# Kernel tuning notes

Measured on AMD Instinct MI355X. Metric: run time of the kernel, lower is better.

The kernel has to match this reference:

```python
import jax, jax.numpy as jnp
import numpy as np

# Conv config matching init_kwargs
C_IN, C_OUT = 128, 256
KH, KW = 3, 3
STRIDE = (1, 1)
PADDING = ((1, 1), (1, 1))
DILATION = (1, 1)
B, H, W = 32, 56, 56


def setup_inputs() -> dict:
    key = jax.random.key(0)
    k1, k2, k3 = jax.random.split(key, 3)
    x = jax.random.normal(k1, (B, C_IN, H, W), dtype=jnp.float32)
    # Flattened weight as stored by Conv2DUF: conv.weight.view(O,-1).t() -> [C*kh*kw, O]
    weight = jax.random.normal(k2, (C_IN * KH * KW, C_OUT), dtype=jnp.float32) * 0.02
    bias = jax.random.normal(k3, (C_OUT,), dtype=jnp.float32) * 0.02
    return {"x": x, "weight": weight, "bias": bias}


def reference(x, weight, bias):
    # Conv2DUF computes unfold(x) @ weight + bias, which is exactly a 2D
    # cross-correlation with the original conv kernel. Recover the [O,C,kh,kw]
    # kernel from the flattened [C*kh*kw, O] matrix and use the fused conv
    # primitive (same math, no giant im2col buffer).
    kernel = weight.T.reshape(C_OUT, C_IN, KH, KW)
    out = jax.lax.conv_general_dilated(
        x, kernel,
        window_strides=STRIDE,
        padding=PADDING,
        rhs_dilation=DILATION,
        dimension_numbers=("NCHW", "OIHW", "NCHW"),
    )
    return out + bias[None, :, None, None]
```

## Files before the change

kernel.cpp:

```cpp
#include <hip/hip_runtime.h>
#include <stdint.h>


#define C_INQ 128
#define C_OUTQ 256
#define HDIM 56
#define WDIM 56
#define BDIM 32
#define HP 58
#define WP 58
#define HWPIX (HDIM * WDIM)
#define GSTRIDE (BDIM * HP * WP * 8)
#define XT_ELEMS ((size_t)16 * GSTRIDE)
#define XT_BYTES (XT_ELEMS * 2)

typedef __bf16 bf16x8 __attribute__((ext_vector_type(8)));
typedef unsigned short ushort8 __attribute__((ext_vector_type(8)));
typedef float floatx4 __attribute__((ext_vector_type(4)));

__device__ __forceinline__ unsigned short f2bf(float f) {
  union { float f; unsigned int u; } v; v.f = f;
  unsigned int u = v.u;
  unsigned int r = u + 0x7FFFu + ((u >> 16) & 1u);
  return (unsigned short)(r >> 16);
}
__device__ __forceinline__ unsigned int pack2(float a, float b) {
  return (unsigned int)f2bf(a) | ((unsigned int)f2bf(b) << 16);
}

__global__ __launch_bounds__(256) void pad_transpose_kernel(
    const float* __restrict__ x, unsigned short* __restrict__ xt) {
  const int blk = blockIdx.x;
  const int b = blk / HP;
  const int hp = blk - b * HP;
  const int t = threadIdx.x;
  uint4* __restrict__ xt4 = (uint4*)xt;
  if (hp == 0 || hp == HP - 1) {
    for (int i = t; i < 16 * WP; i += 256) {
      int g = i / WP, wp = i - g * WP;
      xt4[((size_t)(g * BDIM + b) * HP + hp) * WP + wp] = make_uint4(0, 0, 0, 0);
    }
    return;
  }
  const int h = hp - 1;
  if (t < 224) {
    const int g = t / 14;
    const int w4 = (t - g * 14) * 4;
    const float* xp = x + ((size_t)b * C_INQ + g * 8) * HWPIX + h * WDIM + w4;
    float4 L0 = *(const float4*)(xp);
    float4 L1 = *(const float4*)(xp + HWPIX);
    float4 L2 = *(const float4*)(xp + 2 * HWPIX);
    float4 L3 = *(const float4*)(xp + 3 * HWPIX);
    float4 L4 = *(const float4*)(xp + 4 * HWPIX);
    float4 L5 = *(const float4*)(xp + 5 * HWPIX);
    float4 L6 = *(const float4*)(xp + 6 * HWPIX);
    float4 L7 = *(const float4*)(xp + 7 * HWPIX);
    uint4* dst = xt4 + ((size_t)(g * BDIM + b) * HP + hp) * WP + 1 + w4;
    dst[0] = make_uint4(pack2(L0.x, L1.x), pack2(L2.x, L3.x),
                        pack2(L4.x, L5.x), pack2(L6.x, L7.x));
    dst[1] = make_uint4(pack2(L0.y, L1.y), pack2(L2.y, L3.y),
                        pack2(L4.y, L5.y), pack2(L6.y, L7.y));
    dst[2] = make_uint4(pack2(L0.z, L1.z), pack2(L2.z, L3.z),
                        pack2(L4.z, L5.z), pack2(L6.z, L7.z));
    dst[3] = make_uint4(pack2(L0.w, L1.w), pack2(L2.w, L3.w),
                        pack2(L4.w, L5.w), pack2(L6.w, L7.w));
  } else {
    const int r = t - 224;
    const int g = r >> 1;
    const int wp = (r & 1) * (WP - 1);
    xt4[((size_t)(g * BDIM + b) * HP + hp) * WP + wp] = make_uint4(0, 0, 0, 0);
  }
}

__global__ __launch_bounds__(256) void weight_transform_kernel(
    const float* __restrict__ w, unsigned short* __restrict__ wt) {
  const int bx = blockIdx.x;
  const int khw = bx >> 4;
  const int r4 = bx & 15;
  const int n0w = (r4 >> 2) * 64;
  const int c32 = (r4 & 3) * 32;
  const int t = threadIdx.x;
  __shared__ float lds[32 * 66];
#pragma unroll
  for (int r = 0; r < 8; ++r) {
    int idx = r * 256 + t;
    int n = idx & 63, c = idx >> 6;
    lds[c * 66 + n] = w[(size_t)((c32 + c) * 9 + khw) * C_OUTQ + n0w + n];
  }
  __syncthreads();
  {
    int n = t >> 2, c8 = (t & 3) * 8;
    const float* s = lds + c8 * 66 + n;
    uint4 o;
    o.x = pack2(s[0],   s[66]);
    o.y = pack2(s[132], s[198]);
    o.z = pack2(s[264], s[330]);
    o.w = pack2(s[396], s[462]);
    *(uint4*)(wt + (size_t)khw * (C_OUTQ * C_INQ) + (size_t)(n0w + n) * C_INQ + c32 + c8) = o;
  }
}

#define BM 128
#define BN 256
#define BK 32
#define STEPS 36

__global__ __launch_bounds__(256, 2) void conv_gemm_kernel(
    const unsigned short* __restrict__ xt,
    const unsigned short* __restrict__ wt,
    const float* __restrict__ bias,
    float* __restrict__ out) {
  __shared__ __align__(16) unsigned short ldsA[3 * BM * BK];
  __shared__ __align__(16) unsigned short ldsB[3 * BN * BK];

  const int t = threadIdx.x;
  const int lane = t & 63;
  const int wave = t >> 6;
  const int tile_m = blockIdx.x;

  int gbaseA[2], gbaseB[4];
#pragma unroll
  for (int r = 0; r < 2; ++r) {
    int g = r * 256 + t;
    int row = g >> 2;
    int kpart = (g & 3) ^ (row & 3);
    int pix = tile_m * BM + row;
    int b = pix / HWPIX;
    int p = pix - b * HWPIX;
    int h = p / WDIM;
    int w = p - h * WDIM;
    gbaseA[r] = kpart * GSTRIDE + ((b * HP + h) * WP + w) * 8;
  }
#pragma unroll
  for (int r = 0; r < 4; ++r) {
    int g = r * 256 + t;
    int row = g >> 2;
    int kpart = (g & 3) ^ (row & 3);
    gbaseB[r] = row * C_INQ + kpart * 8;
  }

  const int wm = (wave >> 1) * 64;
  const int wn = (wave & 1) * 128;
  const int mrow = lane & 15;
  const int quad = lane >> 4;

  int aoff[4], boff[8];
#pragma unroll
  for (int i = 0; i < 4; ++i) {
    int row = wm + i * 16 + mrow;
    aoff[i] = row * BK + ((quad ^ (row & 3)) * 8);
  }
#pragma unroll
  for (int j = 0; j < 8; ++j) {
    int row = wn + j * 16 + mrow;
    boff[j] = row * BK + ((quad ^ (row & 3)) * 8);
  }

  const int ldst = wave * 64 * 8;

  floatx4 acc[4][8] = {};

  auto stage = [&](int s2, int bufc) {
    const int khw = s2 >> 2;
    const int cq = s2 & 3;
    const int kh = khw / 3;
    const int kw = khw - kh * 3;
    const int koffA = cq * 4 * GSTRIDE + (kh * WP + kw) * 8;
    const int koffB = khw * (C_OUTQ * C_INQ) + cq * 32;
#pragma unroll
    for (int r = 0; r < 2; ++r)
      __builtin_amdgcn_global_load_lds(
          (const __attribute__((address_space(1))) unsigned int*)(xt + gbaseA[r] + koffA),
          (__attribute__((address_space(3))) unsigned int*)(ldsA + bufc * (BM * BK) + r * 2048 + ldst),
          16, 0, 0);
#pragma unroll
    for (int r = 0; r < 4; ++r)
      __builtin_amdgcn_global_load_lds(
          (const __attribute__((address_space(1))) unsigned int*)(wt + gbaseB[r] + koffB),
          (__attribute__((address_space(3))) unsigned int*)(ldsB + bufc * (BN * BK) + r * 2048 + ldst),
          16, 0, 0);
  };

  auto compute_step = [&](int bufc) {
    const unsigned short* A = ldsA + bufc * (BM * BK);
    const unsigned short* B = ldsB + bufc * (BN * BK);
    bf16x8 afr[4], bfr[8];
#pragma unroll
    for (int i = 0; i < 4; ++i)
      afr[i] = __builtin_bit_cast(bf16x8, *(const ushort8*)(A + aoff[i]));
#pragma unroll
    for (int j = 0; j < 8; ++j)
      bfr[j] = __builtin_bit_cast(bf16x8, *(const ushort8*)(B + boff[j]));
#pragma unroll
    for (int i = 0; i < 4; ++i)
#pragma unroll
      for (int j = 0; j < 8; ++j)
        acc[i][j] = __builtin_amdgcn_mfma_f32_16x16x32_bf16(afr[i], bfr[j], acc[i][j], 0, 0, 0);
  };

#define K_STEP(S, BUF, VM, DOSTAGE)                                  \
  {                                                                  \
    asm volatile("s_waitcnt vmcnt(" VM ")" ::: "memory");            \
    __builtin_amdgcn_s_barrier();                                    \
    compute_step(BUF);                                               \
    __builtin_amdgcn_s_barrier();                                    \
    if (DOSTAGE) stage((S) + 3, BUF);                                \
  }

  stage(0, 0);
  stage(1, 1);
  stage(2, 2);

#pragma unroll 1
  for (int so = 0; so < 11; ++so) {
    const int s = so * 3;
    K_STEP(s, 0, "12", true);
    K_STEP(s + 1, 1, "12", true);
    K_STEP(s + 2, 2, "12", true);
  }
  K_STEP(33, 0, "12", false);
  K_STEP(34, 1, "6", false);
  K_STEP(35, 2, "0", false);
#undef K_STEP

  float bv[8];
#pragma unroll
  for (int jn = 0; jn < 8; ++jn) bv[jn] = bias[wn + jn * 16 + mrow];
#pragma unroll
  for (int i = 0; i < 4; ++i) {
    const int mbase = tile_m * BM + wm + i * 16 + quad * 4;
    const int b = mbase / HWPIX;
    const int p = mbase - b * HWPIX;
    float* obase = out + (size_t)b * (C_OUTQ * HWPIX) + p;
#pragma unroll
    for (int jn = 0; jn < 8; ++jn) {
      const int ng = wn + jn * 16 + mrow;
      floatx4 v = acc[i][jn];
      v[0] += bv[jn]; v[1] += bv[jn]; v[2] += bv[jn]; v[3] += bv[jn];
      *(floatx4*)(obase + (size_t)ng * HWPIX) = v;
    }
  }
}

extern "C" void kernel_launch(void* const* d_in, const int* in_sizes, int n_in,
                              void* d_out, int out_size, void* d_ws, size_t ws_size,
                              hipStream_t stream) {
  const float* x    = (const float*)d_in[0];
  const float* w    = (const float*)d_in[1];
  const float* bias = (const float*)d_in[2];
  float* out = (float*)d_out;

  unsigned short* xt = (unsigned short*)d_ws;
  unsigned short* wt = (unsigned short*)((char*)d_ws + XT_BYTES);

  hipLaunchKernelGGL(pad_transpose_kernel, dim3(BDIM * HP), dim3(256), 0, stream, x, xt);
  hipLaunchKernelGGL(weight_transform_kernel, dim3(144), dim3(256), 0, stream, w, wt);
  hipLaunchKernelGGL(conv_gemm_kernel, dim3(784), dim3(256), 0, stream, xt, wt, bias, out);
}
```

Baseline: 234.4 us.

## Enlarge GEMM tile to 256x256x64 with 8 waves and merge prep kernels

New measurement: 232.1 us. Within noise of the previous version (-1.0%).

```diff
diff --git a/kernel.cpp b/kernel.cpp
--- a/kernel.cpp
+++ b/kernel.cpp
@@ -28,102 +28,102 @@
   return (unsigned int)f2bf(a) | ((unsigned int)f2bf(b) << 16);
 }
 
-__global__ __launch_bounds__(256) void pad_transpose_kernel(
-    const float* __restrict__ x, unsigned short* __restrict__ xt) {
-  const int blk = blockIdx.x;
-  const int b = blk / HP;
-  const int hp = blk - b * HP;
+#define PAD_BLOCKS (BDIM * HP)
+__global__ __launch_bounds__(256) void prep_kernel(
+    const float* __restrict__ x, unsigned short* __restrict__ xt,
+    const float* __restrict__ w, unsigned short* __restrict__ wt) {
   const int t = threadIdx.x;
-  uint4* __restrict__ xt4 = (uint4*)xt;
-  if (hp == 0 || hp == HP - 1) {
-    for (int i = t; i < 16 * WP; i += 256) {
-      int g = i / WP, wp = i - g * WP;
+  if (blockIdx.x < PAD_BLOCKS) {
+    const int blk = blockIdx.x;
+    const int b = blk / HP;
+    const int hp = blk - b * HP;
+    uint4* __restrict__ xt4 = (uint4*)xt;
+    if (hp == 0 || hp == HP - 1) {
+      for (int i = t; i < 16 * WP; i += 256) {
+        int g = i / WP, wp = i - g * WP;
+        xt4[((size_t)(g * BDIM + b) * HP + hp) * WP + wp] = make_uint4(0, 0, 0, 0);
+      }
+      return;
+    }
+    const int h = hp - 1;
+    if (t < 224) {
+      const int g = t / 14;
+      const int w4 = (t - g * 14) * 4;
+      const float* xp = x + ((size_t)b * C_INQ + g * 8) * HWPIX + h * WDIM + w4;
+      float4 L0 = *(const float4*)(xp);
+      float4 L1 = *(const float4*)(xp + HWPIX);
+      float4 L2 = *(const float4*)(xp + 2 * HWPIX);
+      float4 L3 = *(const float4*)(xp + 3 * HWPIX);
+      float4 L4 = *(const float4*)(xp + 4 * HWPIX);
+      float4 L5 = *(const float4*)(xp + 5 * HWPIX);
+      float4 L6 = *(const float4*)(xp + 6 * HWPIX);
+      float4 L7 = *(const float4*)(xp + 7 * HWPIX);
+      uint4* dst = xt4 + ((size_t)(g * BDIM + b) * HP + hp) * WP + 1 + w4;
+      dst[0] = make_uint4(pack2(L0.x, L1.x), pack2(L2.x, L3.x),
+                          pack2(L4.x, L5.x), pack2(L6.x, L7.x));
+      dst[1] = make_uint4(pack2(L0.y, L1.y), pack2(L2.y, L3.y),
+                          pack2(L4.y, L5.y), pack2(L6.y, L7.y));
+      dst[2] = make_uint4(pack2(L0.z, L1.z), pack2(L2.z, L3.z),
+                          pack2(L4.z, L5.z), pack2(L6.z, L7.z));
+      dst[3] = make_uint4(pack2(L0.w, L1.w), pack2(L2.w, L3.w),
+                          pack2(L4.w, L5.w), pack2(L6.w, L7.w));
+    } else {
+      const int r = t - 224;
+      const int g = r >> 1;
+      const int wp = (r & 1) * (WP - 1);
       xt4[((size_t)(g * BDIM + b) * HP + hp) * WP + wp] = make_uint4(0, 0, 0, 0);
     }
-    return;
-  }
-  const int h = hp - 1;
-  if (t < 224) {
-    const int g = t / 14;
-    const int w4 = (t - g * 14) * 4;
-    const float* xp = x + ((size_t)b * C_INQ + g * 8) * HWPIX + h * WDIM + w4;
-    float4 L0 = *(const float4*)(xp);
-    float4 L1 = *(const float4*)(xp + HWPIX);
-    float4 L2 = *(const float4*)(xp + 2 * HWPIX);
-    float4 L3 = *(const float4*)(xp + 3 * HWPIX);
-    float4 L4 = *(const float4*)(xp + 4 * HWPIX);
-    float4 L5 = *(const float4*)(xp + 5 * HWPIX);
-    float4 L6 = *(const float4*)(xp + 6 * HWPIX);
-    float4 L7 = *(const float4*)(xp + 7 * HWPIX);
-    uint4* dst = xt4 + ((size_t)(g * BDIM + b) * HP + hp) * WP + 1 + w4;
-    dst[0] = make_uint4(pack2(L0.x, L1.x), pack2(L2.x, L3.x),
-                        pack2(L4.x, L5.x), pack2(L6.x, L7.x));
-    dst[1] = make_uint4(pack2(L0.y, L1.y), pack2(L2.y, L3.y),
-                        pack2(L4.y, L5.y), pack2(L6.y, L7.y));
-    dst[2] = make_uint4(pack2(L0.z, L1.z), pack2(L2.z, L3.z),
-                        pack2(L4.z, L5.z), pack2(L6.z, L7.z));
-    dst[3] = make_uint4(pack2(L0.w, L1.w), pack2(L2.w, L3.w),
-                        pack2(L4.w, L5.w), pack2(L6.w, L7.w));
   } else {
-    const int r = t - 224;
-    const int g = r >> 1;
-    const int wp = (r & 1) * (WP - 1);
-    xt4[((size_t)(g * BDIM + b) * HP + hp) * WP + wp] = make_uint4(0, 0, 0, 0);
-  }
-}
-
-__global__ __launch_bounds__(256) void weight_transform_kernel(
-    const float* __restrict__ w, unsigned short* __restrict__ wt) {
-  const int bx = blockIdx.x;
-  const int khw = bx >> 4;
-  const int r4 = bx & 15;
-  const int n0w = (r4 >> 2) * 64;
-  const int c32 = (r4 & 3) * 32;
-  const int t = threadIdx.x;
-  __shared__ float lds[32 * 66];
-#pragma unroll
-  for (int r = 0; r < 8; ++r) {
-    int idx = r * 256 + t;
-    int n = idx & 63, c = idx >> 6;
-    lds[c * 66 + n] = w[(size_t)((c32 + c) * 9 + khw) * C_OUTQ + n0w + n];
-  }
-  __syncthreads();
-  {
-    int n = t >> 2, c8 = (t & 3) * 8;
-    const float* s = lds + c8 * 66 + n;
-    uint4 o;
-    o.x = pack2(s[0],   s[66]);
-    o.y = pack2(s[132], s[198]);
-    o.z = pack2(s[264], s[330]);
-    o.w = pack2(s[396], s[462]);
-    *(uint4*)(wt + (size_t)khw * (C_OUTQ * C_INQ) + (size_t)(n0w + n) * C_INQ + c32 + c8) = o;
-  }
-}
-
-#define BM 128
+    const int bx = blockIdx.x - PAD_BLOCKS;
+    const int khw = bx >> 4;
+    const int r4 = bx & 15;
+    const int n0w = (r4 >> 2) * 64;
+    const int c32 = (r4 & 3) * 32;
+    __shared__ float lds[32 * 66];
+#pragma unroll
+    for (int r = 0; r < 8; ++r) {
+      int idx = r * 256 + t;
+      int n = idx & 63, c = idx >> 6;
+      lds[c * 66 + n] = w[(size_t)((c32 + c) * 9 + khw) * C_OUTQ + n0w + n];
+    }
+    __syncthreads();
+    {
+      int n = t >> 2, c8 = (t & 3) * 8;
+      const float* s = lds + c8 * 66 + n;
+      uint4 o;
+      o.x = pack2(s[0],   s[66]);
+      o.y = pack2(s[132], s[198]);
+      o.z = pack2(s[264], s[330]);
+      o.w = pack2(s[396], s[462]);
+      *(uint4*)(wt + (size_t)khw * (C_OUTQ * C_INQ) + (size_t)(n0w + n) * C_INQ + c32 + c8) = o;
+    }
+  }
+}
+
+#define BM 256
 #define BN 256
-#define BK 32
-#define STEPS 36
-
-__global__ __launch_bounds__(256, 2) void conv_gemm_kernel(
+#define BK 64
+#define NT 18
+
+__global__ __launch_bounds__(512, 2) void conv_gemm_kernel(
     const unsigned short* __restrict__ xt,
     const unsigned short* __restrict__ wt,
     const float* __restrict__ bias,
     float* __restrict__ out) {
-  __shared__ __align__(16) unsigned short ldsA[3 * BM * BK];
-  __shared__ __align__(16) unsigned short ldsB[3 * BN * BK];
+  __shared__ __align__(16) unsigned short ldsA[2 * BM * BK];
+  __shared__ __align__(16) unsigned short ldsB[2 * BN * BK];
 
   const int t = threadIdx.x;
   const int lane = t & 63;
   const int wave = t >> 6;
   const int tile_m = blockIdx.x;
 
-  int gbaseA[2], gbaseB[4];
-#pragma unroll
-  for (int r = 0; r < 2; ++r) {
-    int g = r * 256 + t;
-    int row = g >> 2;
-    int kpart = (g & 3) ^ (row & 3);
+  int gbaseA[4], gbaseB[4];
+#pragma unroll
+  for (int r = 0; r < 4; ++r) {
+    int g = r * 512 + t;
+    int row = g >> 3;
+    int kpart = (g & 7) ^ (row & 7);
     int pix = tile_m * BM + row;
     int b = pix / HWPIX;
     int p = pix - b * HWPIX;
@@ -133,110 +133,111 @@
   }
 #pragma unroll
   for (int r = 0; r < 4; ++r) {
-    int g = r * 256 + t;
-    int row = g >> 2;
-    int kpart = (g & 3) ^ (row & 3);
-    gbaseB[r] = row * C_INQ + kpart * 8;
-  }
-
-  const int wm = (wave >> 1) * 64;
-  const int wn = (wave & 1) * 128;
+    int g = r * 512 + t;
+    int n = g >> 3;
+    int kpart = (g & 7) ^ (n & 7);
+    gbaseB[r] = n * C_INQ + kpart * 8;
+  }
+
+  const int wm = (wave >> 2) * 128;
+  const int wn = (wave & 3) * 64;
   const int mrow = lane & 15;
   const int quad = lane >> 4;
-
-  int aoff[4], boff[8];
-#pragma unroll
-  for (int i = 0; i < 4; ++i) {
-    int row = wm + i * 16 + mrow;
-    aoff[i] = row * BK + ((quad ^ (row & 3)) * 8);
-  }
-#pragma unroll
-  for (int j = 0; j < 8; ++j) {
-    int row = wn + j * 16 + mrow;
-    boff[j] = row * BK + ((quad ^ (row & 3)) * 8);
-  }
-
-  const int ldst = wave * 64 * 8;
-
-  floatx4 acc[4][8] = {};
-
-  auto stage = [&](int s2, int bufc) {
-    const int khw = s2 >> 2;
-    const int cq = s2 & 3;
+  const int xorv = mrow & 7;
+  const int kx0 = (quad ^ xorv) * 8;
+  const int kx1 = ((4 + quad) ^ xorv) * 8;
+
+  floatx4 acc[8][4] = {};
+
+  auto stage = [&](int kt, int buf) {
+    const int khw = kt >> 1;
+    const int chalf = kt & 1;
     const int kh = khw / 3;
     const int kw = khw - kh * 3;
-    const int koffA = cq * 4 * GSTRIDE + (kh * WP + kw) * 8;
-    const int koffB = khw * (C_OUTQ * C_INQ) + cq * 32;
-#pragma unroll
-    for (int r = 0; r < 2; ++r)
+    const int koffA = chalf * 8 * GSTRIDE + (kh * WP + kw) * 8;
+    const int koffB = khw * (C_OUTQ * C_INQ) + chalf * 64;
+    const int ldst = t * 8;
+#pragma unroll
+    for (int r = 0; r < 4; ++r)
       __builtin_amdgcn_global_load_lds(
           (const __attribute__((address_space(1))) unsigned int*)(xt + gbaseA[r] + koffA),
-          (__attribute__((address_space(3))) unsigned int*)(ldsA + bufc * (BM * BK) + r * 2048 + ldst),
+          (__attribute__((address_space(3))) unsigned int*)(ldsA + buf * (BM * BK) + r * 4096 + ldst),
           16, 0, 0);
 #pragma unroll
     for (int r = 0; r < 4; ++r)
       __builtin_amdgcn_global_load_lds(
           (const __attribute__((address_space(1))) unsigned int*)(wt + gbaseB[r] + koffB),
-          (__attribute__((address_space(3))) unsigned int*)(ldsB + bufc * (BN * BK) + r * 2048 + ldst),
+          (__attribute__((address_space(3))) unsigned int*)(ldsB + buf * (BN * BK) + r * 4096 + ldst),
           16, 0, 0);
   };
 
-  auto compute_step = [&](int bufc) {
-    const unsigned short* A = ldsA + bufc * (BM * BK);
-    const unsigned short* B = ldsB + bufc * (BN * BK);
-    bf16x8 afr[4], bfr[8];
-#pragma unroll
-    for (int i = 0; i < 4; ++i)
-      afr[i] = __builtin_bit_cast(bf16x8, *(const ushort8*)(A + aoff[i]));
-#pragma unroll
-    for (int j = 0; j < 8; ++j)
-      bfr[j] = __builtin_bit_cast(bf16x8, *(const ushort8*)(B + boff[j]));
-#pragma unroll
-    for (int i = 0; i < 4; ++i)
-#pragma unroll
-      for (int j = 0; j < 8; ++j)
-        acc[i][j] = __builtin_amdgcn_mfma_f32_16x16x32_bf16(afr[i], bfr[j], acc[i][j], 0, 0, 0);
+  auto compute_tile = [&](int buf) {
+    const unsigned short* A = ldsA + buf * (BM * BK);
+    const unsigned short* B = ldsB + buf * (BN * BK);
+    bf16x8 bfr[4][2];
+#pragma unroll
+    for (int j = 0; j < 4; ++j) {
+      const unsigned short* br = B + (wn + j * 16 + mrow) * BK;
+      bfr[j][0] = __builtin_bit_cast(bf16x8, *(const ushort8*)(br + kx0));
+      bfr[j][1] = __builtin_bit_cast(bf16x8, *(const ushort8*)(br + kx1));
+    }
+#pragma unroll
+    for (int p = 0; p < 4; ++p) {
+      bf16x8 af[2][2];
+#pragma unroll
+      for (int i2 = 0; i2 < 2; ++i2) {
+        const unsigned short* ar = A + (wm + (p * 2 + i2) * 16 + mrow) * BK;
+        af[i2][0] = __builtin_bit_cast(bf16x8, *(const ushort8*)(ar + kx0));
+        af[i2][1] = __builtin_bit_cast(bf16x8, *(const ushort8*)(ar + kx1));
+      }
+      __builtin_amdgcn_s_setprio(1);
+#pragma unroll
+      for (int i2 = 0; i2 < 2; ++i2)
+#pragma unroll
+        for (int u = 0; u < 2; ++u)
+#pragma unroll
+          for (int j = 0; j < 4; ++j)
+            acc[p * 2 + i2][j] = __builtin_amdgcn_mfma_f32_16x16x32_bf16(
+                af[i2][u], bfr[j][u], acc[p * 2 + i2][j], 0, 0, 0);
+      __builtin_amdgcn_s_setprio(0);
+    }
   };
 
-#define K_STEP(S, BUF, VM, DOSTAGE)                                  \
+#define K_STEP(T, BUF, VM, DOSTAGE)                                  \
   {                                                                  \
     asm volatile("s_waitcnt vmcnt(" VM ")" ::: "memory");            \
     __builtin_amdgcn_s_barrier();                                    \
-    compute_step(BUF);                                               \
+    compute_tile(BUF);                                               \
     __builtin_amdgcn_s_barrier();                                    \
-    if (DOSTAGE) stage((S) + 3, BUF);                                \
+    if (DOSTAGE) stage((T) + 2, BUF);                                \
   }
 
   stage(0, 0);
   stage(1, 1);
-  stage(2, 2);
 
 #pragma unroll 1
-  for (int so = 0; so < 11; ++so) {
-    const int s = so * 3;
-    K_STEP(s, 0, "12", true);
-    K_STEP(s + 1, 1, "12", true);
-    K_STEP(s + 2, 2, "12", true);
-  }
-  K_STEP(33, 0, "12", false);
-  K_STEP(34, 1, "6", false);
-  K_STEP(35, 2, "0", false);
+  for (int tt = 0; tt < 16; tt += 2) {
+    K_STEP(tt, 0, "8", true);
+    K_STEP(tt + 1, 1, "8", true);
+  }
+  K_STEP(16, 0, "8", false);
+  K_STEP(17, 1, "0", false);
 #undef K_STEP
 
-  float bv[8];
-#pragma unroll
-  for (int jn = 0; jn < 8; ++jn) bv[jn] = bias[wn + jn * 16 + mrow];
-#pragma unroll
-  for (int i = 0; i < 4; ++i) {
+  float bv[4];
+#pragma unroll
+  for (int j = 0; j < 4; ++j) bv[j] = bias[wn + j * 16 + mrow];
+#pragma unroll
+  for (int i = 0; i < 8; ++i) {
     const int mbase = tile_m * BM + wm + i * 16 + quad * 4;
     const int b = mbase / HWPIX;
     const int p = mbase - b * HWPIX;
     float* obase = out + (size_t)b * (C_OUTQ * HWPIX) + p;
 #pragma unroll
-    for (int jn = 0; jn < 8; ++jn) {
-      const int ng = wn + jn * 16 + mrow;
-      floatx4 v = acc[i][jn];
-      v[0] += bv[jn]; v[1] += bv[jn]; v[2] += bv[jn]; v[3] += bv[jn];
+    for (int j = 0; j < 4; ++j) {
+      const int ng = wn + j * 16 + mrow;
+      floatx4 v = acc[i][j];
+      v[0] += bv[j]; v[1] += bv[j]; v[2] += bv[j]; v[3] += bv[j];
       *(floatx4*)(obase + (size_t)ng * HWPIX) = v;
     }
   }
@@ -253,7 +254,8 @@
   unsigned short* xt = (unsigned short*)d_ws;
   unsigned short* wt = (unsigned short*)((char*)d_ws + XT_BYTES);
 
-  hipLaunchKernelGGL(pad_transpose_kernel, dim3(BDIM * HP), dim3(256), 0, stream, x, xt);
-  hipLaunchKernelGGL(weight_transform_kernel, dim3(144), dim3(256), 0, stream, w, wt);
-  hipLaunchKernelGGL(conv_gemm_kernel, dim3(784), dim3(256), 0, stream, xt, wt, bias, out);
-}
+  hipLaunchKernelGGL(prep_kernel, dim3(PAD_BLOCKS + 144), dim3(256), 0, stream,
+                     x, xt, w, wt);
+  hipLaunchKernelGGL(conv_gemm_kernel, dim3(392), dim3(512), 0, stream,
+                     xt, wt, bias, out);
+}
```
